# Kernel tuning notes

Hardware: AMD Instinct MI355X
Metric: run time of the kernel (lower is better)

## Reference

```python
import jax, jax.numpy as jnp
import numpy as np

N_NODES = 50000
N_EDGES = 800000
IN_F = 128
HID = 256
N_CLS = 10
NUM_GRAPHS = 256


def setup_inputs() -> dict:
    key = jax.random.key(0)
    ks = jax.random.split(key, 8)
    x = jax.random.normal(ks[0], (N_NODES, IN_F), dtype=jnp.float32)
    edge_index = jax.random.randint(ks[1], (2, N_EDGES), 0, N_NODES, dtype=jnp.int64)
    batch = jnp.sort(jax.random.randint(ks[2], (N_NODES,), 0, NUM_GRAPHS, dtype=jnp.int64))
    # Glorot-style init for weights (GCNConv default), zeros bias
    W1 = jax.random.normal(ks[3], (IN_F, HID), dtype=jnp.float32) / np.sqrt(IN_F)
    b1 = jnp.zeros((HID,), dtype=jnp.float32)
    W2 = jax.random.normal(ks[4], (HID, HID), dtype=jnp.float32) / np.sqrt(HID)
    b2 = jnp.zeros((HID,), dtype=jnp.float32)
    Wlin = jax.random.normal(ks[5], (HID, N_CLS), dtype=jnp.float32) / np.sqrt(HID)
    blin = jnp.zeros((N_CLS,), dtype=jnp.float32)
    return {"x": x, "edge_index": edge_index, "batch": batch,
            "W1": W1, "b1": b1, "W2": W2, "b2": b2, "Wlin": Wlin, "blin": blin}


def reference(x, edge_index, batch, W1, b1, W2, b2, Wlin, blin):
    N = x.shape[0]
    # PyG GCNConv default: add self-loops, symmetric normalization D^-1/2 A D^-1/2
    loop = jnp.arange(N, dtype=edge_index.dtype)
    src = jnp.concatenate([edge_index[0], loop])  # message source (row)
    dst = jnp.concatenate([edge_index[1], loop])  # aggregation target (col)
    deg = jax.ops.segment_sum(jnp.ones_like(dst, dtype=x.dtype), dst, num_segments=N)
    dinv = jnp.where(deg > 0, jax.lax.rsqrt(deg), 0.0)
    norm = dinv[src] * dinv[dst]  # [E+N]

    def gcn_conv(h, W, b):
        h = h @ W                          # linear transform first (GCNConv)
        msg = h[src] * norm[:, None]       # gather + edge scale
        agg = jax.ops.segment_sum(msg, dst, num_segments=N)  # scatter-add
        return agg + b

    h = jax.nn.relu(gcn_conv(x, W1, b1))
    h = gcn_conv(h, W2, b2)

    # global_mean_pool over batch ids
    counts = jax.ops.segment_sum(jnp.ones((N,), x.dtype), batch, num_segments=NUM_GRAPHS)
    pooled = jax.ops.segment_sum(h, batch, num_segments=NUM_GRAPHS)
    pooled = pooled / jnp.maximum(counts, 1.0)[:, None]  # [NUM_GRAPHS, HID]

    return pooled @ Wlin + blin  # forward returns logits (softmax unused in forward)
```

## Files before the change

kernel.cpp:

```cpp
#include <hip/hip_runtime.h>
#include <hip/hip_bf16.h>

typedef __hip_bfloat16 bf16;
typedef __attribute__((ext_vector_type(8))) short short8;
typedef __attribute__((ext_vector_type(4))) float f32x4;
typedef __attribute__((ext_vector_type(2))) float f32x2;

#define N_NODES 50000
#define N_EDGES 800000
#define IN_F    128
#define HID     256
#define N_CLS   10
#define N_GRAPH 256

#define NB 98
#define PBLOCKS 256

__device__ __forceinline__ int IG(const int* __restrict__ p, int i, int w) {
    return w ? p[2 * i] : p[i];
}
__device__ __forceinline__ float LF(const void* __restrict__ p, int i, int isbf) {
    return isbf ? __bfloat162float(((const bf16*)p)[i]) : ((const float*)p)[i];
}
__device__ __forceinline__ float b2f(unsigned short h) {
    union { unsigned u; float f; } c; c.u = ((unsigned)h) << 16; return c.f;
}
__device__ __forceinline__ unsigned short f2b(float x) {
    bf16 h = __float2bfloat16(x);
    union { bf16 b; unsigned short u; } c; c.b = h; return c.u;
}
__device__ __forceinline__ float f8s(unsigned b) {
    union { unsigned u; float f; } c;
    c.u = ((b & 0x80u) << 24) | ((b & 0x7Fu) << 20);
    return c.f;
}
#define F8SCALE 0x1p120f
__device__ __forceinline__ unsigned f2fp8(float x) {
    unsigned short h = f2b(x * 0x1p-120f);
    unsigned s = ((unsigned)h >> 8) & 0x80u;
    unsigned mag = (unsigned)h & 0x7FFFu;
    unsigned r = (mag + 7u + ((mag >> 4) & 1u)) >> 4;
    if (r > 0x7Eu) r = 0x7Eu;
    return s | r;
}

#if defined(__has_builtin)
#if __has_builtin(__builtin_amdgcn_cvt_pk_f32_fp8)
#define HW_FP8 1
#endif
#if __has_builtin(__builtin_amdgcn_cvt_pk_fp8_f32)
#define HW_FP8E 1
#endif
#endif

__device__ __forceinline__ f32x2 cvt2lo(unsigned v) {
#ifdef HW_FP8
    return __builtin_amdgcn_cvt_pk_f32_fp8((int)v, false);
#else
    f32x2 r; r[0] = f8s(v & 0xFF) * F8SCALE; r[1] = f8s((v >> 8) & 0xFF) * F8SCALE; return r;
#endif
}
__device__ __forceinline__ f32x2 cvt2hi(unsigned v) {
#ifdef HW_FP8
    return __builtin_amdgcn_cvt_pk_f32_fp8((int)v, true);
#else
    f32x2 r; r[0] = f8s((v >> 16) & 0xFF) * F8SCALE; r[1] = f8s(v >> 24) * F8SCALE; return r;
#endif
}
__device__ __forceinline__ unsigned pk4_fp8(float v0, float v1, float v2, float v3) {
#ifdef HW_FP8E
    int o = __builtin_amdgcn_cvt_pk_fp8_f32(v0, v1, 0, false);
    o = __builtin_amdgcn_cvt_pk_fp8_f32(v2, v3, o, true);
    return (unsigned)o;
#else
    return f2fp8(v0) | (f2fp8(v1) << 8) | (f2fp8(v2) << 16) | (f2fp8(v3) << 24);
#endif
}

__global__ __launch_bounds__(256) void k_partA1(const int* __restrict__ ei, int* __restrict__ bucketCnt,
                                                int* __restrict__ blockBase,
                                                const unsigned short* __restrict__ x,
                                                int* __restrict__ flags, int E, int N) {
    int t = threadIdx.x;
    if (blockIdx.x == PBLOCKS) {
        __shared__ int nz, cnt;
        if (t == 0) { nz = 0; cnt = 0; }
        __syncthreads();
        int found = 0, c = 0;
        for (int s = 0; s < 4; ++s) {
            int idx = 2 * (t * 4 + s) + 1;
            if (ei[idx] != 0) found = 1;
        }
        for (int s = 0; s < 8; ++s) {
            unsigned short h = x[t * 8 + s];
            int e = (h >> 7) & 0xFF;
            if (e >= 110 && e <= 135) c++;
        }
        if (found) atomicAdd(&nz, 1);
        atomicAdd(&cnt, c);
        __syncthreads();
        if (t == 0) {
            flags[0] = (nz == 0) ? 1 : 0;
            flags[1] = (cnt > 1536) ? 1 : 0;
        }
        return;
    }
    __shared__ int h[NB];
    __shared__ int wsh;
    if (t == 0) wsh = 0;
    if (t < NB) h[t] = 0;
    __syncthreads();
    int found = 0;
    for (int s = 0; s < 4; ++s) {
        int idx = 2 * (t * 4 + s) + 1;
        if (ei[idx] != 0) found = 1;
    }
    if (found) atomicAdd(&wsh, 1);
    __syncthreads();
    int w = (wsh == 0) ? 1 : 0;
    for (int e = blockIdx.x * 256 + t; e < E; e += PBLOCKS * 256) {
        int d = IG(ei, E + e, w);
        int s = IG(ei, e, w);
        if ((unsigned)d < (unsigned)N && (unsigned)s < (unsigned)N)
            atomicAdd(&h[d >> 9], 1);
    }
    __syncthreads();
    if (t < NB)
        blockBase[blockIdx.x * NB + t] = atomicAdd(&bucketCnt[t * 16], h[t]);
}

__global__ __launch_bounds__(128) void k_bscan(const int* __restrict__ bucketCnt,
                                               int* __restrict__ bucketBase) {
    __shared__ int s[128];
    int t = threadIdx.x;
    int v = (t < NB) ? bucketCnt[t * 16] : 0;
    s[t] = v;
    __syncthreads();
    for (int off = 1; off < 128; off <<= 1) {
        int add = (t >= off) ? s[t - off] : 0;
        __syncthreads();
        s[t] += add;
        __syncthreads();
    }
    if (t <= NB) bucketBase[t] = (t < NB) ? (s[t] - v) : s[NB - 1] + 0;
    if (t == NB - 1) bucketBase[NB] = s[t];
}

__global__ __launch_bounds__(256) void k_partA2(const int* __restrict__ ei,
                                                const int* __restrict__ bucketBase,
                                                const int* __restrict__ blockBase,
                                                unsigned* __restrict__ part,
                                                const int* __restrict__ flags, int E, int N) {
    __shared__ int cur[NB];
    int t = threadIdx.x;
    if (t < NB) cur[t] = bucketBase[t] + blockBase[blockIdx.x * NB + t];
    __syncthreads();
    int w = flags[0];
    for (int e = blockIdx.x * 256 + t; e < E; e += PBLOCKS * 256) {
        int d = IG(ei, E + e, w);
        int s = IG(ei, e, w);
        if ((unsigned)d < (unsigned)N && (unsigned)s < (unsigned)N) {
            int slot = atomicAdd(&cur[d >> 9], 1);
            part[slot] = ((unsigned)(d & 511) << 16) | (unsigned)s;
        }
    }
}

#define PB_W1 98
#define PB_W2 226
#define PB_GB 482
#define PB_TOT 678
__global__ __launch_bounds__(256) void k_partB(const unsigned* __restrict__ part,
                                               const int* __restrict__ bucketBase,
                                               int* __restrict__ rowptr, float* __restrict__ dinv,
                                               int* __restrict__ col,
                                               const void* __restrict__ W1, unsigned short* __restrict__ w1t,
                                               const void* __restrict__ W2, unsigned short* __restrict__ w2t,
                                               const int* __restrict__ batch, int* __restrict__ gstart,
                                               const int* __restrict__ flags, int N) {
    int b = blockIdx.x, t = threadIdx.x;
    if (b >= NB) {
        int fb = flags[1];
        if (b < PB_W2) {
            int i = (b - PB_W1) * 256 + t;
            int n = i >> 7, k = i & 127;
            w1t[i] = f2b(LF(W1, k * 256 + n, fb));
        } else if (b < PB_GB) {
            int i = (b - PB_W2) * 256 + t;
            int n = i >> 8, k = i & 255;
            w2t[i] = f2b(LF(W2, k * 256 + n, fb));
        } else {
            int i = (b - PB_GB) * 256 + t;
            if (i <= N_NODES) {
                int w = flags[0];
                int prev = (i == 0) ? -1 : IG(batch, i - 1, w);
                int cur  = (i == N_NODES) ? N_GRAPH : IG(batch, i, w);
                if (prev < -1) prev = -1;
                if (cur > N_GRAPH) cur = N_GRAPH;
                for (int g = prev + 1; g <= cur; ++g)
                    if (g >= 0 && g <= N_GRAPH) gstart[g] = i;
            }
        }
        return;
    }
    __shared__ int hist[512];
    __shared__ int scn[512];
    __shared__ int pair[256];
    int s0 = bucketBase[b], e0 = bucketBase[b + 1];
    hist[t] = 0; hist[t + 256] = 0;
    __syncthreads();
    for (int j = s0 + t; j < e0; j += 256)
        atomicAdd(&hist[part[j] >> 16], 1);
    __syncthreads();
    int a0 = hist[2 * t], a1 = hist[2 * t + 1];
    int pv = a0 + a1;
    pair[t] = pv;
    __syncthreads();
    for (int off = 1; off < 256; off <<= 1) {
        int add = (t >= off) ? pair[t - off] : 0;
        __syncthreads();
        pair[t] += add;
        __syncthreads();
    }
    int pbase = pair[t] - pv;
    scn[2 * t] = pbase;
    scn[2 * t + 1] = pbase + a0;
    __syncthreads();
#pragma unroll
    for (int hh = 0; hh < 2; ++hh) {
        int l = t + hh * 256;
        int node = b * 512 + l;
        if (node < N) {
            rowptr[node] = s0 + scn[l];
            dinv[node] = rsqrtf((float)(hist[l] + 1));
        }
    }
    if (b == 0 && t == 0) rowptr[N] = bucketBase[NB];
    __syncthreads();
    for (int j = s0 + t; j < e0; j += 256) {
        unsigned p = part[j];
        int pos = s0 + atomicAdd(&scn[p >> 16], 1);
        col[pos] = (int)(p & 0xFFFFu);
    }
}

#define CVTX_BLOCKS 6250
__global__ __launch_bounds__(256) void k_cvt(const void* __restrict__ x, const float* __restrict__ dinv,
                                             unsigned char* __restrict__ xs8,
                                             const int* __restrict__ flags) {
    int fb = flags[1];
    int gid = blockIdx.x * 256 + threadIdx.x;
    int row = gid >> 5;
    float d = dinv[row];
    float vx, vy, vz, vw;
    if (fb) {
        ushort4 v = ((const ushort4*)x)[gid];
        vx = b2f(v.x); vy = b2f(v.y); vz = b2f(v.z); vw = b2f(v.w);
    } else {
        float4 v = ((const float4*)x)[gid];
        vx = v.x; vy = v.y; vz = v.z; vw = v.w;
    }
    ((unsigned*)xs8)[gid] = pk4_fp8(vx * d, vy * d, vz * d, vw * d);
}

__global__ __launch_bounds__(256) void k_gcn2l(const unsigned short* __restrict__ A,
                                               const unsigned short* __restrict__ B1t,
                                               const unsigned short* __restrict__ B2t,
                                               unsigned char* __restrict__ C8, int M,
                                               const float* __restrict__ dinv,
                                               const void* __restrict__ bias1,
                                               const int* __restrict__ flags) {
    __shared__ unsigned short As1[64 * 136];
    __shared__ unsigned short Hs[64 * 264];
    int t = threadIdx.x;
    int lane = t & 63;
    int w = t >> 6;
    int bm = blockIdx.x * 64;
    int l15 = lane & 15, quad = lane >> 4;
    int fb = flags[1];

    {
        const uint4* src = (const uint4*)&A[(size_t)bm * 128];
#pragma unroll
        for (int j = 0; j < 4; ++j) {
            int f = t + j * 256;
            int row = f >> 4, cu = f & 15;
            *(uint4*)&As1[row * 136 + cu * 8] = src[(size_t)row * 16 + cu];
        }
    }
    __syncthreads();

    f32x4 acc[4][4];
#pragma unroll
    for (int ar = 0; ar < 4; ++ar)
#pragma unroll
        for (int tt = 0; tt < 4; ++tt) acc[ar][tt] = (f32x4){0.f, 0.f, 0.f, 0.f};

#pragma unroll
    for (int ks = 0; ks < 4; ++ks) {
        short8 a[4], b[4];
#pragma unroll
        for (int ar = 0; ar < 4; ++ar)
            a[ar] = *(const short8*)&As1[(ar * 16 + l15) * 136 + ks * 32 + quad * 8];
#pragma unroll
        for (int tt = 0; tt < 4; ++tt)
            b[tt] = *(const short8*)&B1t[(size_t)(w * 64 + tt * 16 + l15) * 128 + ks * 32 + quad * 8];
#pragma unroll
        for (int tt = 0; tt < 4; ++tt)
#pragma unroll
            for (int ar = 0; ar < 4; ++ar)
                acc[ar][tt] = __builtin_amdgcn_mfma_f32_16x16x32_bf16(b[tt], a[ar], acc[ar][tt], 0, 0, 0);
    }

    float drow[4];
#pragma unroll
    for (int ar = 0; ar < 4; ++ar) {
        int row = bm + ar * 16 + l15;
        drow[ar] = (row < M) ? dinv[row] : 1.f;
    }
#pragma unroll
    for (int tt = 0; tt < 4; ++tt) {
        int colb = w * 64 + tt * 16 + quad * 4;
        float bc[4];
#pragma unroll
        for (int rr = 0; rr < 4; ++rr) bc[rr] = LF(bias1, colb + rr, fb);
#pragma unroll
        for (int ar = 0; ar < 4; ++ar) {
            ushort4 o;
            o.x = f2b(fmaxf(fmaf(acc[ar][tt][0], drow[ar], bc[0]), 0.f));
            o.y = f2b(fmaxf(fmaf(acc[ar][tt][1], drow[ar], bc[1]), 0.f));
            o.z = f2b(fmaxf(fmaf(acc[ar][tt][2], drow[ar], bc[2]), 0.f));
            o.w = f2b(fmaxf(fmaf(acc[ar][tt][3], drow[ar], bc[3]), 0.f));
            *(ushort4*)&Hs[(ar * 16 + l15) * 264 + colb] = o;
            acc[ar][tt] = (f32x4){0.f, 0.f, 0.f, 0.f};
        }
    }
    __syncthreads();

#pragma unroll
    for (int ks = 0; ks < 8; ++ks) {
        short8 a[4], b[4];
#pragma unroll
        for (int ar = 0; ar < 4; ++ar)
            a[ar] = *(const short8*)&Hs[(ar * 16 + l15) * 264 + ks * 32 + quad * 8];
#pragma unroll
        for (int tt = 0; tt < 4; ++tt)
            b[tt] = *(const short8*)&B2t[(size_t)(w * 64 + tt * 16 + l15) * 256 + ks * 32 + quad * 8];
#pragma unroll
        for (int tt = 0; tt < 4; ++tt)
#pragma unroll
            for (int ar = 0; ar < 4; ++ar)
                acc[ar][tt] = __builtin_amdgcn_mfma_f32_16x16x32_bf16(b[tt], a[ar], acc[ar][tt], 0, 0, 0);
    }

    unsigned* Cs = (unsigned*)As1;
    __syncthreads();
#pragma unroll
    for (int tt = 0; tt < 4; ++tt) {
#pragma unroll
        for (int ar = 0; ar < 4; ++ar) {
            float v0 = acc[ar][tt][0] * drow[ar];
            float v1 = acc[ar][tt][1] * drow[ar];
            float v2 = acc[ar][tt][2] * drow[ar];
            float v3 = acc[ar][tt][3] * drow[ar];
            Cs[(ar * 16 + l15) * 68 + w * 16 + tt * 4 + quad] = pk4_fp8(v0, v1, v2, v3);
        }
    }
    __syncthreads();
    int r = t >> 2, h = t & 3;
    if (bm + r < M) {
        const unsigned* src = Cs + r * 68 + h * 16;
        uint4* dst = (uint4*)&C8[(size_t)(bm + r) * 256 + h * 64];
#pragma unroll
        for (int j = 0; j < 4; ++j) dst[j] = *(const uint4*)(src + j * 4);
    }
}

__global__ __launch_bounds__(256) void k_agg2(const unsigned char* __restrict__ XS,
                                              const int* __restrict__ rowptr, const int* __restrict__ col,
                                              unsigned short* __restrict__ Hout, int N) {
    int jb = blockIdx.x;
    int x8 = jb & 7, k = jb >> 3;
    int gIdx = k >> 4, win = k & 15;
    int node0 = (gIdx * 8 + x8) * 64 + win * 4;
    int lane = threadIdx.x & 63;
    int i = node0 + (threadIdx.x >> 6);
    if (i >= N) return;
    int fo = lane * 2;
    unsigned sv = *(const unsigned short*)&XS[(size_t)i * 128 + fo];
    f32x2 a = cvt2lo(sv);
    int s = rowptr[i], e = rowptr[i + 1];
    int j = s;
    while (j + 16 <= e) {
        unsigned v[16];
#pragma unroll
        for (int q = 0; q < 16; ++q)
            v[q] = *(const unsigned short*)&XS[(size_t)col[j + q] * 128 + fo];
#pragma unroll
        for (int q = 0; q < 16; ++q) a += cvt2lo(v[q]);
        j += 16;
    }
    if (j + 8 <= e) {
        unsigned v[8];
#pragma unroll
        for (int q = 0; q < 8; ++q)
            v[q] = *(const unsigned short*)&XS[(size_t)col[j + q] * 128 + fo];
#pragma unroll
        for (int q = 0; q < 8; ++q) a += cvt2lo(v[q]);
        j += 8;
    }
    if (j + 4 <= e) {
        unsigned v[4];
#pragma unroll
        for (int q = 0; q < 4; ++q)
            v[q] = *(const unsigned short*)&XS[(size_t)col[j + q] * 128 + fo];
#pragma unroll
        for (int q = 0; q < 4; ++q) a += cvt2lo(v[q]);
        j += 4;
    }
    for (; j < e; ++j)
        a += cvt2lo(*(const unsigned short*)&XS[(size_t)col[j] * 128 + fo]);
    ushort2 o;
    o.x = f2b(a[0]); o.y = f2b(a[1]);
    *(ushort2*)&Hout[(size_t)i * 128 + fo] = o;
}

__global__ __launch_bounds__(256) void k_agg4p(const unsigned char* __restrict__ XW,
                                               const int* __restrict__ rowptr, const int* __restrict__ col,
                                               const float* __restrict__ dinv,
                                               const int* __restrict__ batch,
                                               const int* __restrict__ flags,
                                               float* __restrict__ partial,
                                               float* __restrict__ pooledX, int N) {
    __shared__ float red[4][256];
    __shared__ int gs[4];
    int t = threadIdx.x;
    int lane = t & 63, sub = t >> 6;
    int i = blockIdx.x * 4 + sub;
    int fo = lane * 4;
    float v[4] = {0.f, 0.f, 0.f, 0.f};
    int g = -1;
    if (i < N) {
        g = IG(batch, i, flags[0]);
        unsigned sv = *(const unsigned*)&XW[(size_t)i * 256 + fo];
        f32x2 a01 = cvt2lo(sv), a23 = cvt2hi(sv);
        int s = rowptr[i], e = rowptr[i + 1];
        int j = s;
        while (j + 16 <= e) {
            unsigned vv[16];
#pragma unroll
            for (int q = 0; q < 16; ++q)
                vv[q] = *(const unsigned*)&XW[(size_t)col[j + q] * 256 + fo];
#pragma unroll
            for (int q = 0; q < 16; ++q) { a01 += cvt2lo(vv[q]); a23 += cvt2hi(vv[q]); }
            j += 16;
        }
        if (j + 8 <= e) {
            unsigned vv[8];
#pragma unroll
            for (int q = 0; q < 8; ++q)
                vv[q] = *(const unsigned*)&XW[(size_t)col[j + q] * 256 + fo];
#pragma unroll
            for (int q = 0; q < 8; ++q) { a01 += cvt2lo(vv[q]); a23 += cvt2hi(vv[q]); }
            j += 8;
        }
        if (j + 4 <= e) {
            unsigned vv[4];
#pragma unroll
            for (int q = 0; q < 4; ++q)
                vv[q] = *(const unsigned*)&XW[(size_t)col[j + q] * 256 + fo];
#pragma unroll
            for (int q = 0; q < 4; ++q) { a01 += cvt2lo(vv[q]); a23 += cvt2hi(vv[q]); }
            j += 4;
        }
        for (; j < e; ++j) {
            unsigned vv = *(const unsigned*)&XW[(size_t)col[j] * 256 + fo];
            a01 += cvt2lo(vv); a23 += cvt2hi(vv);
        }
        float di = dinv[i];
        v[0] = a01[0] * di; v[1] = a01[1] * di;
        v[2] = a23[0] * di; v[3] = a23[1] * di;
    }
    if (lane == 0) gs[sub] = g;
#pragma unroll
    for (int k2 = 0; k2 < 4; ++k2) red[sub][fo + k2] = v[k2];
    __syncthreads();
    bool uni = (gs[0] >= 0) && gs[0] == gs[1] && gs[1] == gs[2] && gs[2] == gs[3];
    if (uni) {
        float s4 = red[0][t] + red[1][t] + red[2][t] + red[3][t];
        partial[(size_t)blockIdx.x * 256 + t] = s4;
    } else if (g >= 0) {
#pragma unroll
        for (int k2 = 0; k2 < 4; ++k2)
            atomicAdd(&pooledX[g * 256 + fo + k2], v[k2]);
    }
}

__global__ __launch_bounds__(512) void k_poolfinal(const float* __restrict__ partial,
                                                   const float* __restrict__ pooledX,
                                                   const int* __restrict__ gstart,
                                                   const void* __restrict__ b2,
                                                   const void* __restrict__ Wlin,
                                                   const void* __restrict__ blin,
                                                   const int* __restrict__ flags,
                                                   void* __restrict__ outv) {
    __shared__ float red[8][256];
    __shared__ float p[256];
    int g = blockIdx.x, t = threadIdx.x;
    int sub = t >> 6, lane = t & 63;
    int s = gstart[g], e = gstart[g + 1];
    int cnt = e - s;
    int b0 = (s + 3) >> 2, b1 = e >> 2;
    int fo = lane * 4;
    float a0 = 0.f, a1 = 0.f, a2 = 0.f, a3 = 0.f;
    for (int b = b0 + sub; b < b1; b += 8) {
        float4 v = *(const float4*)&partial[(size_t)b * 256 + fo];
        a0 += v.x; a1 += v.y; a2 += v.z; a3 += v.w;
    }
    red[sub][fo + 0] = a0;
    red[sub][fo + 1] = a1;
    red[sub][fo + 2] = a2;
    red[sub][fo + 3] = a3;
    __syncthreads();
    int fb = flags[1];
    if (t < 256) {
        float sum8 = pooledX[g * 256 + t];
#pragma unroll
        for (int q = 0; q < 8; ++q) sum8 += red[q][t];
        float inv = 1.f / fmaxf((float)cnt, 1.f);
        float bb = (cnt > 0) ? LF(b2, t, fb) : 0.f;
        p[t] = sum8 * inv + bb;
    }
    __syncthreads();
    if (t < N_CLS) {
        float sum = LF(blin, t, fb);
        for (int f = 0; f < HID; ++f) sum = fmaf(p[f], LF(Wlin, f * N_CLS + t, fb), sum);
        if (fb) ((bf16*)outv)[g * N_CLS + t] = __float2bfloat16(sum);
        else    ((float*)outv)[g * N_CLS + t] = sum;
    }
}

extern "C" void kernel_launch(void* const* d_in, const int* in_sizes, int n_in,
                              void* d_out, int out_size, void* d_ws, size_t ws_size,
                              hipStream_t stream) {
    (void)n_in; (void)ws_size; (void)in_sizes; (void)out_size;
    const void* x     = d_in[0];
    const int*  ei    = (const int*)d_in[1];
    const int*  batch = (const int*)d_in[2];
    const void* W1    = d_in[3];
    const void* b1    = d_in[4];
    const void* W2    = d_in[5];
    const void* b2    = d_in[6];
    const void* Wl    = d_in[7];
    const void* bl    = d_in[8];

    const int N = N_NODES, E = N_EDGES, F = IN_F, H = HID, G = N_GRAPH;

    char* ws = (char*)d_ws;
    size_t off = 0;
    auto alloc = [&](size_t bytes) -> void* {
        void* p = ws + off;
        off += (bytes + 511) & ~(size_t)511;
        return p;
    };
    unsigned char*  xs8  = (unsigned char*)alloc((size_t)N * F);
    unsigned short* aggX = (unsigned short*)alloc((size_t)N * F * 2);
    unsigned char*  XW2s8 = (unsigned char*)alloc((size_t)N * H);
    float*          partial = (float*)alloc((size_t)(N / 4) * H * 4);
    float*          pooledX = (float*)alloc((size_t)G * H * 4);
    unsigned short* w1t  = (unsigned short*)alloc((size_t)H * F * 2);
    unsigned short* w2t  = (unsigned short*)alloc((size_t)H * H * 2);
    int*   bucketCnt = (int*)alloc((size_t)NB * 16 * 4);
    int*   bucketBase = (int*)alloc((size_t)(NB + 1) * 4);
    int*   blockBase = (int*)alloc((size_t)PBLOCKS * NB * 4);
    unsigned* part  = (unsigned*)alloc((size_t)E * 4);
    int*   gstart  = (int*)alloc((size_t)(G + 1) * 4);
    float* dinv    = (float*)alloc((size_t)N * 4);
    int*   rowptr  = (int*)alloc((size_t)(N + 1) * 4);
    int*   flags   = (int*)alloc(512);
    int*   col     = (int*)alloc((size_t)E * 4);
    size_t zero_bytes = (size_t)NB * 16 * 4;

    hipMemsetAsync(bucketCnt, 0, zero_bytes, stream);
    hipMemsetAsync(pooledX, 0, (size_t)G * H * 4, stream);

    k_partA1<<<PBLOCKS + 1, 256, 0, stream>>>(ei, bucketCnt, blockBase,
                                              (const unsigned short*)x, flags, E, N);
    k_bscan<<<1, 128, 0, stream>>>(bucketCnt, bucketBase);
    k_partA2<<<PBLOCKS, 256, 0, stream>>>(ei, bucketBase, blockBase, part, flags, E, N);
    k_partB<<<PB_TOT, 256, 0, stream>>>(part, bucketBase, rowptr, dinv, col,
                                        W1, w1t, W2, w2t, batch, gstart, flags, N);
    k_cvt<<<CVTX_BLOCKS, 256, 0, stream>>>(x, dinv, xs8, flags);

    int g64 = (N + 63) >> 6;
    int aggBlocks = ((g64 + 7) >> 3) * 8 * 16;
    int nbAgg = (N + 3) / 4;

    k_agg2<<<aggBlocks, 256, 0, stream>>>(xs8, rowptr, col, aggX, N);
    k_gcn2l<<<g64, 256, 0, stream>>>(aggX, w1t, w2t, XW2s8, N, dinv, b1, flags);
    k_agg4p<<<nbAgg, 256, 0, stream>>>(XW2s8, rowptr, col, dinv, batch, flags, partial, pooledX, N);
    k_poolfinal<<<G, 512, 0, stream>>>(partial, pooledX, gstart, b2, Wl, bl, flags, d_out);
}
```

Baseline: 251.7 us.

## Defer second GCN weight matmul past aggregation and pooling via linearity

Since layer-2 aggregation and mean pooling are linear, the W2 multiply is moved from the per-node GEMM (50000x256x256) to after pooling (256 graphs x 256x256) inside the final kernel. The first-layer kernel now writes relu(h1)*dinv directly as fp8 and drops its second MFMA stage and shared buffer. This removes most of the layer-2 GEMM FLOPs in exchange for a scalar per-thread 256-length dot product in the pooling kernel. Results change slightly in rounding, because fp8 quantisation now applies to H1 rather than to H1·W2.

New measurement: 242.6 us. 1.04x faster.

```diff
diff --git a/kernel.cpp b/kernel.cpp
--- a/kernel.cpp
+++ b/kernel.cpp
@@ -263,15 +263,13 @@
     ((unsigned*)xs8)[gid] = pk4_fp8(vx * d, vy * d, vz * d, vw * d);
 }
 
-__global__ __launch_bounds__(256) void k_gcn2l(const unsigned short* __restrict__ A,
-                                               const unsigned short* __restrict__ B1t,
-                                               const unsigned short* __restrict__ B2t,
-                                               unsigned char* __restrict__ C8, int M,
-                                               const float* __restrict__ dinv,
-                                               const void* __restrict__ bias1,
-                                               const int* __restrict__ flags) {
+__global__ __launch_bounds__(256) void k_gcn1(const unsigned short* __restrict__ A,
+                                              const unsigned short* __restrict__ B1t,
+                                              unsigned char* __restrict__ C8, int M,
+                                              const float* __restrict__ dinv,
+                                              const void* __restrict__ bias1,
+                                              const int* __restrict__ flags) {
     __shared__ unsigned short As1[64 * 136];
-    __shared__ unsigned short Hs[64 * 264];
     int t = threadIdx.x;
     int lane = t & 63;
     int w = t >> 6;
@@ -318,6 +316,8 @@
         int row = bm + ar * 16 + l15;
         drow[ar] = (row < M) ? dinv[row] : 1.f;
     }
+    __syncthreads();
+    unsigned* Cs = (unsigned*)As1;
 #pragma unroll
     for (int tt = 0; tt < 4; ++tt) {
         int colb = w * 64 + tt * 16 + quad * 4;
@@ -326,43 +326,10 @@
         for (int rr = 0; rr < 4; ++rr) bc[rr] = LF(bias1, colb + rr, fb);
 #pragma unroll
         for (int ar = 0; ar < 4; ++ar) {
-            ushort4 o;
-            o.x = f2b(fmaxf(fmaf(acc[ar][tt][0], drow[ar], bc[0]), 0.f));
-            o.y = f2b(fmaxf(fmaf(acc[ar][tt][1], drow[ar], bc[1]), 0.f));
-            o.z = f2b(fmaxf(fmaf(acc[ar][tt][2], drow[ar], bc[2]), 0.f));
-            o.w = f2b(fmaxf(fmaf(acc[ar][tt][3], drow[ar], bc[3]), 0.f));
-            *(ushort4*)&Hs[(ar * 16 + l15) * 264 + colb] = o;
-            acc[ar][tt] = (f32x4){0.f, 0.f, 0.f, 0.f};
-        }
-    }
-    __syncthreads();
-
-#pragma unroll
-    for (int ks = 0; ks < 8; ++ks) {
-        short8 a[4], b[4];
-#pragma unroll
-        for (int ar = 0; ar < 4; ++ar)
-            a[ar] = *(const short8*)&Hs[(ar * 16 + l15) * 264 + ks * 32 + quad * 8];
-#pragma unroll
-        for (int tt = 0; tt < 4; ++tt)
-            b[tt] = *(const short8*)&B2t[(size_t)(w * 64 + tt * 16 + l15) * 256 + ks * 32 + quad * 8];
-#pragma unroll
-        for (int tt = 0; tt < 4; ++tt)
-#pragma unroll
-            for (int ar = 0; ar < 4; ++ar)
-                acc[ar][tt] = __builtin_amdgcn_mfma_f32_16x16x32_bf16(b[tt], a[ar], acc[ar][tt], 0, 0, 0);
-    }
-
-    unsigned* Cs = (unsigned*)As1;
-    __syncthreads();
-#pragma unroll
-    for (int tt = 0; tt < 4; ++tt) {
-#pragma unroll
-        for (int ar = 0; ar < 4; ++ar) {
-            float v0 = acc[ar][tt][0] * drow[ar];
-            float v1 = acc[ar][tt][1] * drow[ar];
-            float v2 = acc[ar][tt][2] * drow[ar];
-            float v3 = acc[ar][tt][3] * drow[ar];
+            float v0 = fmaxf(fmaf(acc[ar][tt][0], drow[ar], bc[0]), 0.f) * drow[ar];
+            float v1 = fmaxf(fmaf(acc[ar][tt][1], drow[ar], bc[1]), 0.f) * drow[ar];
+            float v2 = fmaxf(fmaf(acc[ar][tt][2], drow[ar], bc[2]), 0.f) * drow[ar];
+            float v3 = fmaxf(fmaf(acc[ar][tt][3], drow[ar], bc[3]), 0.f) * drow[ar];
             Cs[(ar * 16 + l15) * 68 + w * 16 + tt * 4 + quad] = pk4_fp8(v0, v1, v2, v3);
         }
     }
@@ -499,6 +466,7 @@
 __global__ __launch_bounds__(512) void k_poolfinal(const float* __restrict__ partial,
                                                    const float* __restrict__ pooledX,
                                                    const int* __restrict__ gstart,
+                                                   const unsigned short* __restrict__ w2t,
                                                    const void* __restrict__ b2,
                                                    const void* __restrict__ Wlin,
                                                    const void* __restrict__ blin,
@@ -506,6 +474,7 @@
                                                    void* __restrict__ outv) {
     __shared__ float red[8][256];
     __shared__ float p[256];
+    __shared__ float q[256];
     int g = blockIdx.x, t = threadIdx.x;
     int sub = t >> 6, lane = t & 63;
     int s = gstart[g], e = gstart[g + 1];
@@ -526,15 +495,26 @@
     if (t < 256) {
         float sum8 = pooledX[g * 256 + t];
 #pragma unroll
-        for (int q = 0; q < 8; ++q) sum8 += red[q][t];
+        for (int qq = 0; qq < 8; ++qq) sum8 += red[qq][t];
         float inv = 1.f / fmaxf((float)cnt, 1.f);
-        float bb = (cnt > 0) ? LF(b2, t, fb) : 0.f;
-        p[t] = sum8 * inv + bb;
+        p[t] = sum8 * inv;
+    }
+    __syncthreads();
+    if (t < 256) {
+        float acc2 = (cnt > 0) ? LF(b2, t, fb) : 0.f;
+        const unsigned short* wr = &w2t[(size_t)t * 256];
+        for (int k = 0; k < 256; k += 8) {
+            short8 v8 = *(const short8*)&wr[k];
+#pragma unroll
+            for (int j = 0; j < 8; ++j)
+                acc2 = fmaf(p[k + j], b2f((unsigned short)v8[j]), acc2);
+        }
+        q[t] = acc2;
     }
     __syncthreads();
     if (t < N_CLS) {
         float sum = LF(blin, t, fb);
-        for (int f = 0; f < HID; ++f) sum = fmaf(p[f], LF(Wlin, f * N_CLS + t, fb), sum);
+        for (int f = 0; f < HID; ++f) sum = fmaf(q[f], LF(Wlin, f * N_CLS + t, fb), sum);
         if (fb) ((bf16*)outv)[g * N_CLS + t] = __float2bfloat16(sum);
         else    ((float*)outv)[g * N_CLS + t] = sum;
     }
@@ -565,7 +545,7 @@
     };
     unsigned char*  xs8  = (unsigned char*)alloc((size_t)N * F);
     unsigned short* aggX = (unsigned short*)alloc((size_t)N * F * 2);
-    unsigned char*  XW2s8 = (unsigned char*)alloc((size_t)N * H);
+    unsigned char*  H1s8 = (unsigned char*)alloc((size_t)N * H);
     float*          partial = (float*)alloc((size_t)(N / 4) * H * 4);
     float*          pooledX = (float*)alloc((size_t)G * H * 4);
     unsigned short* w1t  = (unsigned short*)alloc((size_t)H * F * 2);
@@ -597,7 +577,7 @@
     int nbAgg = (N + 3) / 4;
 
     k_agg2<<<aggBlocks, 256, 0, stream>>>(xs8, rowptr, col, aggX, N);
-    k_gcn2l<<<g64, 256, 0, stream>>>(aggX, w1t, w2t, XW2s8, N, dinv, b1, flags);
-    k_agg4p<<<nbAgg, 256, 0, stream>>>(XW2s8, rowptr, col, dinv, batch, flags, partial, pooledX, N);
-    k_poolfinal<<<G, 512, 0, stream>>>(partial, pooledX, gstart, b2, Wl, bl, flags, d_out);
-}
+    k_gcn1<<<g64, 256, 0, stream>>>(aggX, w1t, H1s8, N, dinv, b1, flags);
+    k_agg4p<<<nbAgg, 256, 0, stream>>>(H1s8, rowptr, col, dinv, batch, flags, partial, pooledX, N);
+    k_poolfinal<<<G, 512, 0, stream>>>(partial, pooledX, gstart, w2t, b2, Wl, bl, flags, d_out);
+}
```
